# Performance work log

Hardware: AMD Instinct MI355X
Metric: run time of the kernel (lower is better)

## Reference

```python
import jax, jax.numpy as jnp
import numpy as np

N, IN_CAPS, OUT_CAPS, IN_LEN, OUT_LEN = 64, 256, 128, 16, 32
NUM_ITERATIONS = 3


def _squash(t, axis=-1):
    # scale * t / sqrt(||t||^2) with scale = ||t||^2 / (1 + ||t||^2)
    sq = jnp.sum(t * t, axis=axis, keepdims=True)
    return (sq / (1.0 + sq)) * t / jnp.sqrt(sq)


def setup_inputs() -> dict:
    key = jax.random.key(0)
    k1, k2 = jax.random.split(key)
    x = jax.random.normal(k1, (N, IN_CAPS, IN_LEN), dtype=jnp.float32)
    weight = jax.random.normal(k2, (OUT_CAPS, IN_CAPS, IN_LEN, OUT_LEN), dtype=jnp.float32)
    return {"x": x, "weight": weight}


def reference(x, weight):
    # priors: [out_caps, N, in_caps, out_len]  (torch keeps an extra singleton dim)
    priors = jnp.einsum('nik,oikl->onil', x, weight)
    logits = jnp.zeros_like(priors)
    outputs = None
    for i in range(NUM_ITERATIONS):
        # torch softmax(dim=2) == softmax over the in_caps axis
        probs = jax.nn.softmax(logits, axis=2)
        s = jnp.sum(probs * priors, axis=2, keepdims=True)  # [O, N, 1, L]
        outputs = _squash(s, axis=-1)
        if i != NUM_ITERATIONS - 1:
            # delta broadcasts over out_len, as in the torch code
            logits = logits + jnp.sum(priors * outputs, axis=-1, keepdims=True)
    # squeeze routing dim, transpose to [N, out_caps, out_len]
    return jnp.transpose(outputs[:, :, 0, :], (1, 0, 2))
```

## Files before the change

### kernel.cpp

```cpp
#include <hip/hip_runtime.h>


#define ICAPS 256
#define OCAPS 128
#define WS_XC 67108864ull
#define WS_NEED 68157440ull
#define KPAD 20

typedef __attribute__((ext_vector_type(8))) short s16x8;
typedef __attribute__((ext_vector_type(16))) float f32x16;

union u4s8 { unsigned u[4]; s16x8 v; };

__device__ inline unsigned rne_adj(unsigned u) {
    return u + 0x7FFFu + ((u >> 16) & 1u);
}

__device__ inline void split8(const float* f, s16x8& hi, s16x8& lo) {
    u4s8 H, L;
    #pragma unroll
    for (int c = 0; c < 4; ++c) {
        const unsigned u0 = __float_as_uint(f[2 * c]);
        const unsigned u1 = __float_as_uint(f[2 * c + 1]);
        const unsigned r0 = rne_adj(u0), r1 = rne_adj(u1);
        H.u[c] = __builtin_amdgcn_perm(r1, r0, 0x07060302u);
        const float h0 = __uint_as_float(r0 & 0xFFFF0000u);
        const float h1 = __uint_as_float(r1 & 0xFFFF0000u);
        const unsigned l0 = rne_adj(__float_as_uint(f[2 * c] - h0));
        const unsigned l1 = rne_adj(__float_as_uint(f[2 * c + 1] - h1));
        L.u[c] = __builtin_amdgcn_perm(l1, l0, 0x07060302u);
    }
    hi = H.v; lo = L.v;
}

__global__ __launch_bounds__(512)
void caps_prep(const float* __restrict__ x, const float* __restrict__ w,
               unsigned char* __restrict__ ws) {
    __shared__ float T[8][32 * KPAD];
    const int wv = threadIdx.x >> 6, lane = threadIdx.x & 63;
    const int gid = blockIdx.x * 8 + wv;
    float f[8];
    s16x8 hi, lo;

    if (gid < 32768) {
        const float* src = w + (size_t)gid * 512 + lane * 8;
        const float4 a = *(const float4*)src;
        const float4 b = *(const float4*)(src + 4);
        const float v[8] = {a.x, a.y, a.z, a.w, b.x, b.y, b.z, b.w};
        {
            float* Tw = &T[wv][0];
            const int k = lane >> 2, l0 = (lane & 3) * 8;
            #pragma unroll
            for (int j = 0; j < 8; ++j) Tw[(l0 + j) * KPAD + k] = v[j];
        }
        __syncthreads();
        {
            const float* rd = &T[wv][(lane & 31) * KPAD + (lane >> 5) * 8];
            const float4 ra = *(const float4*)rd;
            const float4 rb = *(const float4*)(rd + 4);
            f[0] = ra.x; f[1] = ra.y; f[2] = ra.z; f[3] = ra.w;
            f[4] = rb.x; f[5] = rb.y; f[6] = rb.z; f[7] = rb.w;
        }
        split8(f, hi, lo);
        s16x8* WC = (s16x8*)ws;
        WC[(size_t)gid * 128 + lane] = hi;
        WC[(size_t)gid * 128 + 64 + lane] = lo;
    } else if (gid < 33280) {
        const int id = gid - 32768;
        const int nh = id >> 8, i = id & 255;
        const int n = lane & 31, kb = (lane >> 5) * 8;
        const float* src = x + ((size_t)(nh * 32 + n) * ICAPS + i) * 16 + kb;
        const float4 a = *(const float4*)src;
        const float4 b = *(const float4*)(src + 4);
        f[0] = a.x; f[1] = a.y; f[2] = a.z; f[3] = a.w;
        f[4] = b.x; f[5] = b.y; f[6] = b.z; f[7] = b.w;
        split8(f, hi, lo);
        s16x8* XC = (s16x8*)(ws + WS_XC);
        XC[(size_t)id * 128 + lane] = hi;
        XC[(size_t)id * 128 + 64 + lane] = lo;
    }
}

__global__ __launch_bounds__(512)
void caps_main(const unsigned char* __restrict__ ws, float* __restrict__ out) {
    __shared__ float lg[ICAPS * 32];
    __shared__ float slab[8 * 1280];
    __shared__ float svv[32 * 33];
    __shared__ float zz[8 * 32];
    __shared__ float zinv[32];

    const int t = threadIdx.x, wv = t >> 6, lane = t & 63;
    const int o = blockIdx.x & 127, nh = blockIdx.x >> 7;
    const int n = lane & 31, half = lane >> 5;

    const s16x8* Wp = (const s16x8*)ws + (size_t)o * ICAPS * 128 + lane;
    const s16x8* Xp = (const s16x8*)(ws + WS_XC) + (size_t)nh * ICAPS * 128 + lane;

    float vr[16];
    const int ibase = wv * 32;

    for (int pass = 0; pass < 3; ++pass) {
        float uacc[16];
        #pragma unroll
        for (int r = 0; r < 16; ++r) uacc[r] = 0.f;
        float z = 0.f;

        s16x8 C[8], Nx[8];
        {
            const size_t b0 = (size_t)ibase * 128;
            C[0] = Wp[b0];       C[1] = Wp[b0 + 64];
            C[2] = Xp[b0];       C[3] = Xp[b0 + 64];
            C[4] = Wp[b0 + 128]; C[5] = Wp[b0 + 192];
            C[6] = Xp[b0 + 128]; C[7] = Xp[b0 + 192];
        }

        if (pass == 0) {
            f32x16 Pa = {}, Pb = {};
            for (int bb = 0; bb < 16; ++bb) {
                if (bb < 15) {
                    const size_t bn = (size_t)(ibase + 2 * (bb + 1)) * 128;
                    Nx[0] = Wp[bn];       Nx[1] = Wp[bn + 64];
                    Nx[2] = Xp[bn];       Nx[3] = Xp[bn + 64];
                    Nx[4] = Wp[bn + 128]; Nx[5] = Wp[bn + 192];
                    Nx[6] = Xp[bn + 128]; Nx[7] = Xp[bn + 192];
                }
                Pa = __builtin_amdgcn_mfma_f32_32x32x16_bf16(C[1], C[2], Pa, 0, 0, 0);
                Pb = __builtin_amdgcn_mfma_f32_32x32x16_bf16(C[5], C[6], Pb, 0, 0, 0);
                Pa = __builtin_amdgcn_mfma_f32_32x32x16_bf16(C[0], C[3], Pa, 0, 0, 0);
                Pb = __builtin_amdgcn_mfma_f32_32x32x16_bf16(C[4], C[7], Pb, 0, 0, 0);
                Pa = __builtin_amdgcn_mfma_f32_32x32x16_bf16(C[0], C[2], Pa, 0, 0, 0);
                Pb = __builtin_amdgcn_mfma_f32_32x32x16_bf16(C[4], C[6], Pb, 0, 0, 0);
                if (bb < 15) {
                    #pragma unroll
                    for (int j = 0; j < 8; ++j) C[j] = Nx[j];
                }
            }
            #pragma unroll
            for (int r = 0; r < 16; ++r) uacc[r] = Pa[r] + Pb[r];
        } else {
            for (int bb = 0; bb < 16; ++bb) {
                if (bb < 15) {
                    const size_t bn = (size_t)(ibase + 2 * (bb + 1)) * 128;
                    Nx[0] = Wp[bn];       Nx[1] = Wp[bn + 64];
                    Nx[2] = Xp[bn];       Nx[3] = Xp[bn + 64];
                    Nx[4] = Wp[bn + 128]; Nx[5] = Wp[bn + 192];
                    Nx[6] = Xp[bn + 128]; Nx[7] = Xp[bn + 192];
                }
                f32x16 P0 = {}, P1 = {};
                P0 = __builtin_amdgcn_mfma_f32_32x32x16_bf16(C[1], C[2], P0, 0, 0, 0);
                P1 = __builtin_amdgcn_mfma_f32_32x32x16_bf16(C[5], C[6], P1, 0, 0, 0);
                P0 = __builtin_amdgcn_mfma_f32_32x32x16_bf16(C[0], C[3], P0, 0, 0, 0);
                P1 = __builtin_amdgcn_mfma_f32_32x32x16_bf16(C[4], C[7], P1, 0, 0, 0);
                P0 = __builtin_amdgcn_mfma_f32_32x32x16_bf16(C[0], C[2], P0, 0, 0, 0);
                P1 = __builtin_amdgcn_mfma_f32_32x32x16_bf16(C[4], C[6], P1, 0, 0, 0);

                #pragma unroll
                for (int j = 0; j < 2; ++j) {
                    const f32x16& P = j ? P1 : P0;
                    const int i = ibase + bb * 2 + j;
                    float da = P[0] * vr[0];
                    float db = P[8] * vr[8];
                    #pragma unroll
                    for (int r = 1; r < 8; ++r) {
                        da = fmaf(P[r], vr[r], da);
                        db = fmaf(P[r + 8], vr[r + 8], db);
                    }
                    float d = da + db;
                    d += __shfl_xor(d, 32);
                    if (pass == 1) {
                        if (half == 0) lg[i * 32 + n] = d;
                    } else {
                        d += lg[i * 32 + n];
                    }
                    const float e = __expf(d);
                    z += e;
                    #pragma unroll
                    for (int r = 0; r < 16; ++r) uacc[r] = fmaf(e, P[r], uacc[r]);
                }
                if (bb < 15) {
                    #pragma unroll
                    for (int j = 0; j < 8; ++j) C[j] = Nx[j];
                }
            }
        }

        #pragma unroll
        for (int c = 0; c < 4; ++c)
            *(float4*)(&slab[wv * 1280 + lane * 20 + c * 4]) =
                make_float4(uacc[4 * c], uacc[4 * c + 1], uacc[4 * c + 2], uacc[4 * c + 3]);
        if (pass > 0 && half == 0) zz[wv * 32 + n] = z;
        __syncthreads();

        #pragma unroll
        for (int hh = 0; hh < 2; ++hh) {
            const int e = t + hh * 512;
            const int lw = e >> 4, r = e & 15;
            float s = 0.f;
            #pragma unroll
            for (int w8 = 0; w8 < 8; ++w8) s += slab[w8 * 1280 + lw * 20 + r];
            const int nn = lw & 31, ll = (r & 3) + 8 * (r >> 2) + 4 * (lw >> 5);
            svv[nn * 33 + ll] = s;
        }
        if (t < 32) {
            if (pass == 0) zinv[t] = 1.0f / 256.0f;
            else {
                float zs = 0.f;
                #pragma unroll
                for (int w8 = 0; w8 < 8; ++w8) zs += zz[w8 * 32 + t];
                zinv[t] = 1.0f / zs;
            }
        }
        __syncthreads();

        {
            const int nq = t >> 4, sub = t & 15;
            const float a = svv[nq * 33 + sub] * zinv[nq];
            const float b = svv[nq * 33 + sub + 16] * zinv[nq];
            float sq = a * a + b * b;
            #pragma unroll
            for (int m = 1; m < 16; m <<= 1) sq += __shfl_xor(sq, m, 16);
            const float sc = sqrtf(sq) / (1.0f + sq);
            if (pass == 2) {
                const int ng = nh * 32 + nq;
                out[((size_t)ng * OCAPS + o) * 32 + sub] = a * sc;
                out[((size_t)ng * OCAPS + o) * 32 + sub + 16] = b * sc;
            } else {
                svv[nq * 33 + sub] = a * sc;
                svv[nq * 33 + sub + 16] = b * sc;
            }
        }
        if (pass < 2) {
            __syncthreads();
            #pragma unroll
            for (int r = 0; r < 16; ++r) {
                const int l = (r & 3) + 8 * (r >> 2) + 4 * half;
                vr[r] = svv[n * 33 + l];
            }
        }
    }
}

#define KLEN  16
#define LLEN  32
#define TN    16
#define LGS   257
#define XROW  20
#define XIST  (TN * XROW + 4)
#define SVS   33
#define RBS   33
#define NSTG  32
#define NSTEP (ICAPS / NSTG)

__global__ __launch_bounds__(512, 2)
void caps_route_fb(const float* __restrict__ xg_all,
                   const float* __restrict__ wg_all,
                   float* __restrict__ out) {
    __shared__ float lg[TN * LGS];
    __shared__ float xt[NSTG * XIST];
    __shared__ float sv[TN * SVS];
    __shared__ float zz[8][TN];
    __shared__ float zinv[TN];

    const int t   = threadIdx.x;
    const int o   = blockIdx.x & 127;
    const int n0  = (blockIdx.x >> 7) * TN;
    const int isp = t >> 4;
    const int lb  = (t >> 2) & 3;
    const int nb  = t & 3;
    const int l0  = lb * 8;

    const float* xg = xg_all + (size_t)n0 * ICAPS * KLEN;
    const float* wg = wg_all + (size_t)o * ICAPS * KLEN * LLEN;

    for (int pass = 0; pass < 3; ++pass) {
        float u[4][8];
        float zq[4] = {0.f, 0.f, 0.f, 0.f};
        #pragma unroll
        for (int q = 0; q < 4; ++q)
            #pragma unroll
            for (int r = 0; r < 8; ++r) u[q][r] = 0.f;

        for (int st = 0; st < NSTEP; ++st) {
            const int i0 = st * NSTG;
            __syncthreads();
            #pragma unroll
            for (int j = 0; j < 4; ++j) {
                const int g   = j * 512 + t;
                const int nn  = g >> 7;
                const int rem = g & 127;
                const int il  = rem >> 2;
                const int k4c = rem & 3;
                *(float4*)(&xt[il * XIST + nn * XROW + k4c * 4]) =
                    *(const float4*)(xg + (size_t)(nn * ICAPS + i0 + il) * KLEN + k4c * 4);
            }
            __syncthreads();

            const int i = i0 + isp;
            const float* wp = wg + (size_t)i * (KLEN * LLEN) + l0;
            const float* xp = &xt[isp * XIST];
            float P[4][8];
            #pragma unroll
            for (int q = 0; q < 4; ++q)
                #pragma unroll
                for (int r = 0; r < 8; ++r) P[q][r] = 0.f;

            #pragma unroll
            for (int k4 = 0; k4 < 4; ++k4) {
                float xq[4][4];
                #pragma unroll
                for (int q = 0; q < 4; ++q)
                    *(float4*)(&xq[q][0]) = *(const float4*)(xp + (nb + 4 * q) * XROW + k4 * 4);
                #pragma unroll
                for (int kk = 0; kk < 4; ++kk) {
                    const int k = k4 * 4 + kk;
                    const float4 wa = *(const float4*)(wp + k * LLEN);
                    const float4 wb = *(const float4*)(wp + k * LLEN + 4);
                    #pragma unroll
                    for (int q = 0; q < 4; ++q) {
                        const float xv = xq[q][kk];
                        P[q][0] = fmaf(xv, wa.x, P[q][0]);
                        P[q][1] = fmaf(xv, wa.y, P[q][1]);
                        P[q][2] = fmaf(xv, wa.z, P[q][2]);
                        P[q][3] = fmaf(xv, wa.w, P[q][3]);
                        P[q][4] = fmaf(xv, wb.x, P[q][4]);
                        P[q][5] = fmaf(xv, wb.y, P[q][5]);
                        P[q][6] = fmaf(xv, wb.z, P[q][6]);
                        P[q][7] = fmaf(xv, wb.w, P[q][7]);
                    }
                }
            }

            if (pass == 0) {
                #pragma unroll
                for (int q = 0; q < 4; ++q)
                    #pragma unroll
                    for (int r = 0; r < 8; ++r) u[q][r] += P[q][r];
            } else {
                #pragma unroll
                for (int q = 0; q < 4; ++q) {
                    const float* vp = &sv[(nb + 4 * q) * SVS + l0];
                    float d = P[q][0] * vp[0] + P[q][1] * vp[1] + P[q][2] * vp[2] + P[q][3] * vp[3]
                            + P[q][4] * vp[4] + P[q][5] * vp[5] + P[q][6] * vp[6] + P[q][7] * vp[7];
                    d += __shfl_xor(d, 4);
                    d += __shfl_xor(d, 8);
                    float lnew = d;
                    if (pass == 2) lnew += lg[(nb + 4 * q) * LGS + i];
                    else if (lb == 0) lg[(nb + 4 * q) * LGS + i] = lnew;
                    const float e = __expf(lnew);
                    zq[q] += e;
                    #pragma unroll
                    for (int r = 0; r < 8; ++r) u[q][r] = fmaf(e, P[q][r], u[q][r]);
                }
            }
        }

        #pragma unroll
        for (int q = 0; q < 4; ++q) {
            #pragma unroll
            for (int r = 0; r < 8; ++r) {
                float v = u[q][r];
                v += __shfl_xor(v, 16);
                v += __shfl_xor(v, 32);
                u[q][r] = v;
            }
            float zv = zq[q];
            zv += __shfl_xor(zv, 16);
            zv += __shfl_xor(zv, 32);
            zq[q] = zv;
        }
        __syncthreads();
        {
            const int wvv = t >> 6, lane = t & 63;
            if (lane < 16) {
                float* rb = &xt[wvv * (16 * RBS) + lane * RBS];
                #pragma unroll
                for (int q = 0; q < 4; ++q)
                    #pragma unroll
                    for (int r = 0; r < 8; ++r) rb[q * 8 + r] = u[q][r];
            }
            if (pass > 0 && lane < 4) {
                #pragma unroll
                for (int q = 0; q < 4; ++q) zz[wvv][lane + 4 * q] = zq[q];
            }
        }
        __syncthreads();
        {
            const int low4 = t >> 5, qr = t & 31;
            const int qq = qr >> 3, rr = qr & 7;
            const int lbb = low4 >> 2, nbb = low4 & 3;
            float ssum = 0.f;
            #pragma unroll
            for (int w8 = 0; w8 < 8; ++w8) ssum += xt[w8 * (16 * RBS) + low4 * RBS + qr];
            sv[(nbb + 4 * qq) * SVS + lbb * 8 + rr] = ssum;
        }
        if (t < TN) {
            if (pass == 0) zinv[t] = 1.0f / 256.0f;
            else {
                float zs = 0.f;
                #pragma unroll
                for (int w8 = 0; w8 < 8; ++w8) zs += zz[w8][t];
                zinv[t] = 1.0f / zs;
            }
        }
        __syncthreads();
        {
            const int nn = t >> 5, l = t & 31;
            const float val = sv[nn * SVS + l] * zinv[nn];
            float sq = val * val;
            #pragma unroll
            for (int m = 1; m < 32; m <<= 1) sq += __shfl_xor(sq, m, 32);
            const float sc = sqrtf(sq) / (1.0f + sq);
            if (pass == 2)
                out[((size_t)(n0 + nn) * OCAPS + o) * LLEN + l] = val * sc;
            else
                sv[nn * SVS + l] = val * sc;
        }
    }
}

extern "C" void kernel_launch(void* const* d_in, const int* in_sizes, int n_in,
                              void* d_out, int out_size, void* d_ws, size_t ws_size,
                              hipStream_t stream) {
    const float* x = (const float*)d_in[0];
    const float* w = (const float*)d_in[1];
    float* outp = (float*)d_out;
    if (ws_size >= WS_NEED) {
        caps_prep<<<dim3(4160), dim3(512), 0, stream>>>(x, w, (unsigned char*)d_ws);
        caps_main<<<dim3(256), dim3(512), 0, stream>>>((const unsigned char*)d_ws, outp);
    } else {
        caps_route_fb<<<dim3(512), dim3(512), 0, stream>>>(x, w, outp);
    }
}
```

Before: 143.7 us.

## Double caps_main block to 1024 threads with 16 waves splitting in_caps

The main routing kernel now runs 16 waves per block, each handling 16 input capsules instead of 32. The 8-register double-buffered prefetch is replaced by a lighter A/B ping-pong that loads one capsule ahead, and the cross-wave reduction is widened to 16 slabs. In the prep kernel, the block-wide barrier is replaced by a wave-local LDS waitcnt, since each wave only uses its own transpose tile. The aim is more latency hiding on the 256-block grid, at the cost of more LDS, register pressure capped by the 1024-thread launch bound, and a longer reduction.

```diff
diff --git a/kernel.cpp b/kernel.cpp
--- a/kernel.cpp
+++ b/kernel.cpp
@@ -53,7 +53,7 @@
             #pragma unroll
             for (int j = 0; j < 8; ++j) Tw[(l0 + j) * KPAD + k] = v[j];
         }
-        __syncthreads();
+        asm volatile("s_waitcnt lgkmcnt(0)" ::: "memory");
         {
             const float* rd = &T[wv][(lane & 31) * KPAD + (lane >> 5) * 8];
             const float4 ra = *(const float4*)rd;
@@ -81,12 +81,43 @@
     }
 }
 
-__global__ __launch_bounds__(512)
+
+#define MF(a, b, c) __builtin_amdgcn_mfma_f32_32x32x16_bf16(a, b, c, 0, 0, 0)
+
+#define LDFRAG(W0, W1, X0, X1, ii)                   \
+    {                                                \
+        const size_t b_ = (size_t)(ii) * 128;        \
+        W0 = Wp[b_]; W1 = Wp[b_ + 64];               \
+        X0 = Xp[b_]; X1 = Xp[b_ + 64];               \
+    }
+
+#define SOFTSTEP(P, ii)                                                   \
+    {                                                                     \
+        float da = P[0] * vr[0], db = P[8] * vr[8];                       \
+        _Pragma("unroll")                                                 \
+        for (int r = 1; r < 8; ++r) {                                     \
+            da = fmaf(P[r], vr[r], da);                                   \
+            db = fmaf(P[r + 8], vr[r + 8], db);                           \
+        }                                                                 \
+        float d = da + db;                                                \
+        d += __shfl_xor(d, 32);                     \
+        if (pass == 1) {                                                  \
+            if (half == 0) lg[(ii) * 32 + n] = d;                         \
+        } else {                                                          \
+            d += lg[(ii) * 32 + n];                                       \
+        }                                                                 \
+        const float e = __expf(d);                                        \
+        z += e;                                                           \
+        _Pragma("unroll")                                                 \
+        for (int r = 0; r < 16; ++r) uacc[r] = fmaf(e, P[r], uacc[r]);    \
+    }
+
+__global__ __launch_bounds__(1024)
 void caps_main(const unsigned char* __restrict__ ws, float* __restrict__ out) {
     __shared__ float lg[ICAPS * 32];
-    __shared__ float slab[8 * 1280];
+    __shared__ float slab[16 * 1280];
     __shared__ float svv[32 * 33];
-    __shared__ float zz[8 * 32];
+    __shared__ float zz[16 * 32];
     __shared__ float zinv[32];
 
     const int t = threadIdx.x, wv = t >> 6, lane = t & 63;
@@ -97,7 +128,7 @@
     const s16x8* Xp = (const s16x8*)(ws + WS_XC) + (size_t)nh * ICAPS * 128 + lane;
 
     float vr[16];
-    const int ibase = wv * 32;
+    const int ibase = wv * 16;
 
     for (int pass = 0; pass < 3; ++pass) {
         float uacc[16];
@@ -105,82 +136,39 @@
         for (int r = 0; r < 16; ++r) uacc[r] = 0.f;
         float z = 0.f;
 
-        s16x8 C[8], Nx[8];
-        {
-            const size_t b0 = (size_t)ibase * 128;
-            C[0] = Wp[b0];       C[1] = Wp[b0 + 64];
-            C[2] = Xp[b0];       C[3] = Xp[b0 + 64];
-            C[4] = Wp[b0 + 128]; C[5] = Wp[b0 + 192];
-            C[6] = Xp[b0 + 128]; C[7] = Xp[b0 + 192];
-        }
+        s16x8 Aw0, Aw1, Ax0, Ax1, Bw0, Bw1, Bx0, Bx1;
+        LDFRAG(Aw0, Aw1, Ax0, Ax1, ibase);
 
         if (pass == 0) {
             f32x16 Pa = {}, Pb = {};
-            for (int bb = 0; bb < 16; ++bb) {
-                if (bb < 15) {
-                    const size_t bn = (size_t)(ibase + 2 * (bb + 1)) * 128;
-                    Nx[0] = Wp[bn];       Nx[1] = Wp[bn + 64];
-                    Nx[2] = Xp[bn];       Nx[3] = Xp[bn + 64];
-                    Nx[4] = Wp[bn + 128]; Nx[5] = Wp[bn + 192];
-                    Nx[6] = Xp[bn + 128]; Nx[7] = Xp[bn + 192];
-                }
-                Pa = __builtin_amdgcn_mfma_f32_32x32x16_bf16(C[1], C[2], Pa, 0, 0, 0);
-                Pb = __builtin_amdgcn_mfma_f32_32x32x16_bf16(C[5], C[6], Pb, 0, 0, 0);
-                Pa = __builtin_amdgcn_mfma_f32_32x32x16_bf16(C[0], C[3], Pa, 0, 0, 0);
-                Pb = __builtin_amdgcn_mfma_f32_32x32x16_bf16(C[4], C[7], Pb, 0, 0, 0);
-                Pa = __builtin_amdgcn_mfma_f32_32x32x16_bf16(C[0], C[2], Pa, 0, 0, 0);
-                Pb = __builtin_amdgcn_mfma_f32_32x32x16_bf16(C[4], C[6], Pb, 0, 0, 0);
-                if (bb < 15) {
-                    #pragma unroll
-                    for (int j = 0; j < 8; ++j) C[j] = Nx[j];
-                }
+            for (int q = 0; q < 8; ++q) {
+                const int iA = ibase + 2 * q;
+                LDFRAG(Bw0, Bw1, Bx0, Bx1, iA + 1);
+                Pa = MF(Aw1, Ax0, Pa);
+                Pa = MF(Aw0, Ax1, Pa);
+                Pa = MF(Aw0, Ax0, Pa);
+                if (q < 7) LDFRAG(Aw0, Aw1, Ax0, Ax1, iA + 2);
+                Pb = MF(Bw1, Bx0, Pb);
+                Pb = MF(Bw0, Bx1, Pb);
+                Pb = MF(Bw0, Bx0, Pb);
             }
             #pragma unroll
             for (int r = 0; r < 16; ++r) uacc[r] = Pa[r] + Pb[r];
         } else {
-            for (int bb = 0; bb < 16; ++bb) {
-                if (bb < 15) {
-                    const size_t bn = (size_t)(ibase + 2 * (bb + 1)) * 128;
-                    Nx[0] = Wp[bn];       Nx[1] = Wp[bn + 64];
-                    Nx[2] = Xp[bn];       Nx[3] = Xp[bn + 64];
-                    Nx[4] = Wp[bn + 128]; Nx[5] = Wp[bn + 192];
-                    Nx[6] = Xp[bn + 128]; Nx[7] = Xp[bn + 192];
-                }
-                f32x16 P0 = {}, P1 = {};
-                P0 = __builtin_amdgcn_mfma_f32_32x32x16_bf16(C[1], C[2], P0, 0, 0, 0);
-                P1 = __builtin_amdgcn_mfma_f32_32x32x16_bf16(C[5], C[6], P1, 0, 0, 0);
-                P0 = __builtin_amdgcn_mfma_f32_32x32x16_bf16(C[0], C[3], P0, 0, 0, 0);
-                P1 = __builtin_amdgcn_mfma_f32_32x32x16_bf16(C[4], C[7], P1, 0, 0, 0);
-                P0 = __builtin_amdgcn_mfma_f32_32x32x16_bf16(C[0], C[2], P0, 0, 0, 0);
-                P1 = __builtin_amdgcn_mfma_f32_32x32x16_bf16(C[4], C[6], P1, 0, 0, 0);
-
-                #pragma unroll
-                for (int j = 0; j < 2; ++j) {
-                    const f32x16& P = j ? P1 : P0;
-                    const int i = ibase + bb * 2 + j;
-                    float da = P[0] * vr[0];
-                    float db = P[8] * vr[8];
-                    #pragma unroll
-                    for (int r = 1; r < 8; ++r) {
-                        da = fmaf(P[r], vr[r], da);
-                        db = fmaf(P[r + 8], vr[r + 8], db);
-                    }
-                    float d = da + db;
-                    d += __shfl_xor(d, 32);
-                    if (pass == 1) {
-                        if (half == 0) lg[i * 32 + n] = d;
-                    } else {
-                        d += lg[i * 32 + n];
-                    }
-                    const float e = __expf(d);
-                    z += e;
-                    #pragma unroll
-                    for (int r = 0; r < 16; ++r) uacc[r] = fmaf(e, P[r], uacc[r]);
-                }
-                if (bb < 15) {
-                    #pragma unroll
-                    for (int j = 0; j < 8; ++j) C[j] = Nx[j];
-                }
+            for (int q = 0; q < 8; ++q) {
+                const int iA = ibase + 2 * q;
+                LDFRAG(Bw0, Bw1, Bx0, Bx1, iA + 1);
+                f32x16 P0 = {};
+                P0 = MF(Aw1, Ax0, P0);
+                P0 = MF(Aw0, Ax1, P0);
+                P0 = MF(Aw0, Ax0, P0);
+                SOFTSTEP(P0, iA);
+                if (q < 7) LDFRAG(Aw0, Aw1, Ax0, Ax1, iA + 2);
+                f32x16 P1 = {};
+                P1 = MF(Bw1, Bx0, P1);
+                P1 = MF(Bw0, Bx1, P1);
+                P1 = MF(Bw0, Bx0, P1);
+                SOFTSTEP(P1, iA + 1);
             }
         }
 
@@ -191,13 +179,11 @@
         if (pass > 0 && half == 0) zz[wv * 32 + n] = z;
         __syncthreads();
 
-        #pragma unroll
-        for (int hh = 0; hh < 2; ++hh) {
-            const int e = t + hh * 512;
-            const int lw = e >> 4, r = e & 15;
+        {
+            const int lw = t >> 4, r = t & 15;
             float s = 0.f;
             #pragma unroll
-            for (int w8 = 0; w8 < 8; ++w8) s += slab[w8 * 1280 + lw * 20 + r];
+            for (int w8 = 0; w8 < 16; ++w8) s += slab[w8 * 1280 + lw * 20 + r];
             const int nn = lw & 31, ll = (r & 3) + 8 * (r >> 2) + 4 * (lw >> 5);
             svv[nn * 33 + ll] = s;
         }
@@ -206,13 +192,13 @@
             else {
                 float zs = 0.f;
                 #pragma unroll
-                for (int w8 = 0; w8 < 8; ++w8) zs += zz[w8 * 32 + t];
+                for (int w8 = 0; w8 < 16; ++w8) zs += zz[w8 * 32 + t];
                 zinv[t] = 1.0f / zs;
             }
         }
         __syncthreads();
 
-        {
+        if (t < 512) {
             const int nq = t >> 4, sub = t & 15;
             const float a = svv[nq * 33 + sub] * zinv[nq];
             const float b = svv[nq * 33 + sub + 16] * zinv[nq];
@@ -426,7 +412,7 @@
     float* outp = (float*)d_out;
     if (ws_size >= WS_NEED) {
         caps_prep<<<dim3(4160), dim3(512), 0, stream>>>(x, w, (unsigned char*)d_ws);
-        caps_main<<<dim3(256), dim3(512), 0, stream>>>((const unsigned char*)d_ws, outp);
+        caps_main<<<dim3(256), dim3(1024), 0, stream>>>((const unsigned char*)d_ws, outp);
     } else {
         caps_route_fb<<<dim3(512), dim3(512), 0, stream>>>(x, w, outp);
     }
```

Result: slower. 570.6 us (+297.1%).
